# Optimization experiments

Hardware: AMD Instinct MI355X
Metric: run time of the kernel (lower is better)

## Reference

```python
import jax, jax.numpy as jnp
import numpy as np

N_TREES, N_LEAVES, PATH_LEN, N_NODES, D, B = 10, 16, 5, 31, 256, 4096


def _local_paths():
    # root-to-leaf paths of a full binary tree, depth 4: 31 nodes, 16 leaves, path len 5
    return np.array([[0, 1 + l // 8, 3 + l // 4, 7 + l // 2, 15 + l]
                     for l in range(N_LEAVES)], np.int32)


def setup_inputs() -> dict:
    key = jax.random.key(0)
    k1, k2, k3, k4, k5, k6 = jax.random.split(key, 6)
    # one activated leaf per tree -> multi-hot cross_features (B, N_TREES*N_LEAVES)
    leaf = jax.random.randint(k1, (B, N_TREES), 0, N_LEAVES)
    cross = jnp.zeros((B, N_TREES, N_LEAVES), jnp.float32)
    cross = cross.at[jnp.arange(B)[:, None], jnp.arange(N_TREES)[None, :], leaf].set(1.0)
    cross_features = cross.reshape(B, N_TREES * N_LEAVES)
    # learned params: node embedding table + single-layer LSTM (torch init scale 1/sqrt(D))
    emb = jax.random.normal(k2, (N_TREES * N_NODES, D), jnp.float32) * 0.02
    s = 1.0 / np.sqrt(D)
    W_ih = jax.random.uniform(k3, (4 * D, D), jnp.float32, -s, s)
    W_hh = jax.random.uniform(k4, (4 * D, D), jnp.float32, -s, s)
    b_ih = jax.random.uniform(k5, (4 * D,), jnp.float32, -s, s)
    b_hh = jax.random.uniform(k6, (4 * D,), jnp.float32, -s, s)
    return {"cross_features": cross_features, "emb": emb, "W_ih": W_ih,
            "W_hh": W_hh, "b_ih": b_ih, "b_hh": b_hh}


def reference(cross_features, emb, W_ih, W_hh, b_ih, b_hh):
    # global path node ids per (tree, leaf): [T, L, P]
    gpaths = jnp.asarray(_local_paths())[None, :, :] + \
        (jnp.arange(N_TREES, dtype=jnp.int32) * N_NODES)[:, None, None]
    # activated leaf per tree (exactly one hot per 16-leaf block)
    leaf = jnp.argmax(cross_features.reshape(B, N_TREES, N_LEAVES), axis=-1)  # [B, T]
    node_ids = gpaths[jnp.arange(N_TREES)[None, :], leaf]                     # [B, T, P]
    x = emb[node_ids].reshape(B * N_TREES, PATH_LEN, D)                       # packed paths
    # precompute input projections for all steps: [N, P, 4D]
    xg = jnp.einsum('npd,gd->npg', x, W_ih) + (b_ih + b_hh)

    def step(carry, xt):
        h, c = carry
        g = xt + h @ W_hh.T
        i, f, gg, o = jnp.split(g, 4, axis=-1)  # torch gate order: i, f, g, o
        c = jax.nn.sigmoid(f) * c + jax.nn.sigmoid(i) * jnp.tanh(gg)
        h = jax.nn.sigmoid(o) * jnp.tanh(c)
        return (h, c), None

    n = B * N_TREES
    h0 = jnp.zeros((n, D), x.dtype)
    (h, _), _ = jax.lax.scan(step, (h0, h0), jnp.swapaxes(xg, 0, 1))
    return h.reshape(B, N_TREES, D)
```

## Files before the change

kernel.cpp:

```cpp
#include <hip/hip_runtime.h>

#define NT 10
#define NL 16
#define NN 31
#define DD 256
#define NB 4096

__device__ unsigned g_gen[NT * 16];

__device__ __forceinline__ float sigf(float x)   { return 1.0f / (1.0f + __expf(-x)); }
__device__ __forceinline__ float tanh_f(float x) { return 2.0f / (1.0f + __expf(-2.0f*x)) - 1.0f; }

__device__ __forceinline__ void pub64(unsigned long long* p, unsigned tag, float v) {
    union { float f; unsigned u; } c; c.f = v;
    __hip_atomic_store(p, ((unsigned long long)tag << 32) | c.u,
                       __ATOMIC_RELAXED, __HIP_MEMORY_SCOPE_AGENT);
}
__device__ __forceinline__ unsigned long long ld64(const unsigned long long* p) {
    return __hip_atomic_load(p, __ATOMIC_RELAXED, __HIP_MEMORY_SCOPE_AGENT);
}
__device__ __forceinline__ float payload(unsigned long long w) {
    union { unsigned u; float f; } c; c.u = (unsigned)w; return c.f;
}

__global__ __launch_bounds__(256) void k_treelstm(
    const float* __restrict__ emb, const float* __restrict__ Wih,
    const float* __restrict__ Whh, const float* __restrict__ bih,
    const float* __restrict__ bhh,
    unsigned long long* __restrict__ hx0, unsigned long long* __restrict__ hx1,
    unsigned long long* __restrict__ hx2, unsigned long long* __restrict__ hx3,
    float* __restrict__ h4g)
{
    __shared__ float es [NN * DD];
    __shared__ float ps [8 * DD];
    __shared__ float xsl[NN * 64];
    __shared__ float hs [8 * DD];
    __shared__ float cbuf[2 * 128];
    __shared__ float bsl[64];
    __shared__ unsigned stag;

    const int tid  = threadIdx.x;
    const int t    = blockIdx.x >> 4;
    const int dt   = blockIdx.x & 15;
    const int kq   = tid >> 6;
    const int w    = tid & 63;
    const int gate = w >> 4;
    const int col  = w & 15;
    const int grow = gate * DD + dt * 16 + col;

    if (tid == 0) {
        unsigned G = __hip_atomic_load(&g_gen[t * 16 + dt],
            __ATOMIC_RELAXED, __HIP_MEMORY_SCOPE_AGENT);
        __hip_atomic_store(&g_gen[t * 16 + dt], G + 1u,
            __ATOMIC_RELAXED, __HIP_MEMORY_SCOPE_AGENT);
        stag = G + 1u;
    }
    if (tid < 64) {
        int g2 = tid >> 4, c3 = tid & 15;
        int r2 = g2 * DD + dt * 16 + c3;
        bsl[tid] = bih[r2] + bhh[r2];
    }

    const float4* Wi4 = (const float4*)Wih + (size_t)grow * 64 + kq * 16;
    const float4* Wh4 = (const float4*)Whh + (size_t)grow * 64 + kq * 16;
    float4 wih[16], whh[16];
    #pragma unroll
    for (int j = 0; j < 16; ++j) { wih[j] = Wi4[j]; whh[j] = Wh4[j]; }

    const float4* emb4 = (const float4*)emb + (size_t)t * NN * 64;
    float4* es4 = (float4*)es;
    #pragma unroll
    for (int r = 0; r < 8; ++r) {
        int idx = tid + 256 * r;
        if (idx < NN * 64) es4[idx] = emb4[idx];
    }
    __syncthreads();
    const unsigned tag = stag;

    auto xbatch = [&](int n0, int nn) {
        __syncthreads();
        float acc[8];
        #pragma unroll
        for (int m = 0; m < 8; ++m) acc[m] = 0.f;
        #pragma unroll
        for (int j = 0; j < 16; ++j) {
            float4 wv = wih[j];
            #pragma unroll
            for (int m = 0; m < 8; ++m) {
                if (m < nn) {
                    float4 h = es4[(n0 + m) * 64 + kq * 16 + j];
                    acc[m] = fmaf(wv.x, h.x, fmaf(wv.y, h.y,
                             fmaf(wv.z, h.z, fmaf(wv.w, h.w, acc[m]))));
                }
            }
        }
        #pragma unroll
        for (int m = 0; m < 8; ++m)
            if (m < nn) ps[m * DD + kq * 64 + w] = acc[m];
        __syncthreads();
        #pragma unroll
        for (int rep = 0; rep < 2; ++rep) {
            int idx = tid + 256 * rep;
            if (idx < nn * 64) {
                int m = idx >> 6, w2 = idx & 63;
                xsl[(n0 + m) * 64 + w2] =
                      ps[m * DD +   0 + w2] + ps[m * DD +  64 + w2]
                    + ps[m * DD + 128 + w2] + ps[m * DD + 192 + w2] + bsl[w2];
            }
        }
        __syncthreads();
    };

    xbatch(0, 1);
    if (tid < 16) {
        float xi  = xsl[ 0 + tid];
        float xgg = xsl[32 + tid];
        float xo  = xsl[48 + tid];
        float c0 = sigf(xi) * tanh_f(xgg);
        float h0 = sigf(xo) * tanh_f(c0);
        cbuf[tid] = c0;
        pub64(hx0 + (size_t)t * DD + dt * 16 + tid, tag, h0);
    }

    xbatch(1, 6);

    {
        const unsigned long long* src = hx0 + (size_t)t * DD;
        unsigned long long v = ld64(src + tid);
        while ((unsigned)(v >> 32) != tag) {
            __builtin_amdgcn_s_sleep(1);
            v = ld64(src + tid);
        }
        hs[tid] = payload(v);
    }
    __syncthreads();

    const unsigned long long* hin[3] = { hx1, hx2, hx3 };
    unsigned long long* hout[3] = { hx1, hx2, hx3 };

    #pragma unroll
    for (int s = 1; s <= 4; ++s) {
        const int L = 1 << (s - 1);

        if (s > 1) {
            const unsigned long long* src = hin[s - 2] + (size_t)t * L * DD;
            unsigned long long v[8];
            #pragma unroll
            for (int r = 0; r < L; ++r) v[r] = ld64(src + tid + 256 * r);
            #pragma unroll
            for (int r = 0; r < L; ++r) {
                while ((unsigned)(v[r] >> 32) != tag) {
                    __builtin_amdgcn_s_sleep(1);
                    v[r] = ld64(src + tid + 256 * r);
                }
                hs[tid + 256 * r] = payload(v[r]);
            }
            __syncthreads();
        }

        const float4* hs4 = (const float4*)hs;
        float acc[8];
        #pragma unroll
        for (int p = 0; p < 8; ++p) acc[p] = 0.f;
        #pragma unroll
        for (int j = 0; j < 16; ++j) {
            float4 wv = whh[j];
            #pragma unroll
            for (int p = 0; p < L; ++p) {
                float4 h = hs4[p * 64 + kq * 16 + j];
                acc[p] = fmaf(wv.x, h.x, fmaf(wv.y, h.y,
                         fmaf(wv.z, h.z, fmaf(wv.w, h.w, acc[p]))));
            }
        }
        #pragma unroll
        for (int p = 0; p < L; ++p) ps[p * DD + kq * 64 + w] = acc[p];
        __syncthreads();

        if (tid < 32 * L) {
            const int p  = tid >> 5;
            const int c2 = tid & 15;
            const int q  = tid >> 4;
            float g0 = 0.f, g1 = 0.f, g2 = 0.f, g3 = 0.f;
            #pragma unroll
            for (int k = 0; k < 4; ++k) {
                const float* pp = ps + p * DD + k * 64;
                g0 += pp[ 0 + c2]; g1 += pp[16 + c2];
                g2 += pp[32 + c2]; g3 += pp[48 + c2];
            }
            const int node = (1 << s) - 1 + q;
            const float* xp = xsl + node * 64;
            float gi = g0 + xp[ 0 + c2];
            float gf = g1 + xp[16 + c2];
            float gg = g2 + xp[32 + c2];
            float go = g3 + xp[48 + c2];
            float cin = cbuf[((s - 1) & 1) * 128 + p * 16 + c2];
            float cn  = sigf(gf) * cin + sigf(gi) * tanh_f(gg);
            float hn  = sigf(go) * tanh_f(cn);
            if (s < 4) {
                cbuf[(s & 1) * 128 + q * 16 + c2] = cn;
                pub64(hout[s - 1] + (size_t)(t * 2 * L + q) * DD
                                  + dt * 16 + c2, tag, hn);
            } else {
                h4g[(size_t)(t * NL + q) * DD + dt * 16 + c2] = hn;
            }
        }

        if (s == 1)      xbatch( 7, 8);
        else if (s == 2) xbatch(15, 8);
        else if (s == 3) xbatch(23, 8);
    }
}

__global__ __launch_bounds__(256) void k_scatter(
    const float* __restrict__ cross, const float* __restrict__ htab,
    float* __restrict__ out)
{
    const int tid  = threadIdx.x;
    const int wave = tid >> 6;
    const int lane = tid & 63;
    const int r0 = (blockIdx.x * 4 + wave) * 4;

    float v = cross[(size_t)r0 * NL + lane];
    unsigned long long m = __ballot(v > 0.5f);

    const int g  = lane >> 4;
    const int rr = r0 + g;
    const int b  = rr / NT;
    const int t  = rr - b * NT;
    unsigned mg = (unsigned)(m >> (g * 16)) & 0xFFFFu;
    int leaf = mg ? (int)__builtin_ctz(mg) : 0;
    int p = t * NL + leaf;

    const float4* h4 = (const float4*)htab;
    float4* o4 = (float4*)out;

    #pragma unroll
    for (int it = 0; it < 4; ++it) {
        int pit = __shfl(p, it * 16);
        o4[(size_t)(r0 + it) * 64 + lane] = h4[(size_t)pit * 64 + lane];
    }
}

extern "C" void kernel_launch(void* const* d_in, const int* in_sizes, int n_in,
                              void* d_out, int out_size, void* d_ws, size_t ws_size,
                              hipStream_t stream)
{
    const float* cross = (const float*)d_in[0];
    const float* emb   = (const float*)d_in[1];
    const float* Wih   = (const float*)d_in[2];
    const float* Whh   = (const float*)d_in[3];
    const float* bih   = (const float*)d_in[4];
    const float* bhh   = (const float*)d_in[5];
    float* out = (float*)d_out;

    unsigned long long* hx0 = (unsigned long long*)d_ws;
    unsigned long long* hx1 = hx0 + (size_t)NT * DD;
    unsigned long long* hx2 = hx1 + (size_t)2 * NT * DD;
    unsigned long long* hx3 = hx2 + (size_t)4 * NT * DD;
    float* h4g = (float*)(hx3 + (size_t)8 * NT * DD);

    hipLaunchKernelGGL(k_treelstm, dim3(160), dim3(256), 0, stream,
                       emb, Wih, Whh, bih, bhh, hx0, hx1, hx2, hx3, h4g);
    hipLaunchKernelGGL(k_scatter, dim3(2560), dim3(256), 0, stream,
                       cross, h4g, out);
}
```

Measured before the change: 100.8 us.

## Fuse leaf scatter into tree-LSTM kernel, overlapping leaf decoding with recurrence

Removes the separate scatter kernel. Each tree-LSTM block now decodes the activated leaf for all 4096 batch rows of its tree, in chunks interleaved with the recurrence steps. After the last step it writes its 16-column slice of the leaf hidden states straight to the output. This drops one launch and the global round-trip of the leaf hidden-state table. In exchange, only 160 blocks write all 42 MB of output, with 64-byte strided stores per row, and every block rereads the cross features for its tree (16 blocks per tree).

```diff
diff --git a/kernel.cpp b/kernel.cpp
--- a/kernel.cpp
+++ b/kernel.cpp
@@ -24,12 +24,12 @@
 }
 
 __global__ __launch_bounds__(256) void k_treelstm(
-    const float* __restrict__ emb, const float* __restrict__ Wih,
-    const float* __restrict__ Whh, const float* __restrict__ bih,
-    const float* __restrict__ bhh,
+    const float* __restrict__ cross, const float* __restrict__ emb,
+    const float* __restrict__ Wih,   const float* __restrict__ Whh,
+    const float* __restrict__ bih,   const float* __restrict__ bhh,
     unsigned long long* __restrict__ hx0, unsigned long long* __restrict__ hx1,
     unsigned long long* __restrict__ hx2, unsigned long long* __restrict__ hx3,
-    float* __restrict__ h4g)
+    float* __restrict__ out)
 {
     __shared__ float es [NN * DD];
     __shared__ float ps [8 * DD];
@@ -37,6 +37,8 @@
     __shared__ float hs [8 * DD];
     __shared__ float cbuf[2 * 128];
     __shared__ float bsl[64];
+    __shared__ float h4f[NL * 16];
+    __shared__ unsigned char leafs[NB];
     __shared__ unsigned stag;
 
     const int tid  = threadIdx.x;
@@ -109,6 +111,28 @@
             }
         }
         __syncthreads();
+    };
+
+    const float4* cf4 = (const float4*)cross;
+    auto leafchunk = [&](int b0) {
+        #pragma unroll
+        for (int r = 0; r < 4; ++r) {
+            int b = b0 + r * 256 + tid;
+            float4 q0 = cf4[(size_t)b * 40 + t * 4 + 0];
+            float4 q1 = cf4[(size_t)b * 40 + t * 4 + 1];
+            float4 q2 = cf4[(size_t)b * 40 + t * 4 + 2];
+            float4 q3 = cf4[(size_t)b * 40 + t * 4 + 3];
+            int lf = 0;
+            if (q3.w > 0.5f) lf = 15; if (q3.z > 0.5f) lf = 14;
+            if (q3.y > 0.5f) lf = 13; if (q3.x > 0.5f) lf = 12;
+            if (q2.w > 0.5f) lf = 11; if (q2.z > 0.5f) lf = 10;
+            if (q2.y > 0.5f) lf =  9; if (q2.x > 0.5f) lf =  8;
+            if (q1.w > 0.5f) lf =  7; if (q1.z > 0.5f) lf =  6;
+            if (q1.y > 0.5f) lf =  5; if (q1.x > 0.5f) lf =  4;
+            if (q0.w > 0.5f) lf =  3; if (q0.z > 0.5f) lf =  2;
+            if (q0.y > 0.5f) lf =  1; if (q0.x > 0.5f) lf =  0;
+            leafs[b] = (unsigned char)lf;
+        }
     };
 
     xbatch(0, 1);
@@ -123,6 +147,7 @@
     }
 
     xbatch(1, 6);
+    leafchunk(0);
 
     {
         const unsigned long long* src = hx0 + (size_t)t * DD;
@@ -201,43 +226,25 @@
                 pub64(hout[s - 1] + (size_t)(t * 2 * L + q) * DD
                                   + dt * 16 + c2, tag, hn);
             } else {
-                h4g[(size_t)(t * NL + q) * DD + dt * 16 + c2] = hn;
-            }
-        }
-
-        if (s == 1)      xbatch( 7, 8);
-        else if (s == 2) xbatch(15, 8);
-        else if (s == 3) xbatch(23, 8);
-    }
-}
-
-__global__ __launch_bounds__(256) void k_scatter(
-    const float* __restrict__ cross, const float* __restrict__ htab,
-    float* __restrict__ out)
-{
-    const int tid  = threadIdx.x;
-    const int wave = tid >> 6;
-    const int lane = tid & 63;
-    const int r0 = (blockIdx.x * 4 + wave) * 4;
-
-    float v = cross[(size_t)r0 * NL + lane];
-    unsigned long long m = __ballot(v > 0.5f);
-
-    const int g  = lane >> 4;
-    const int rr = r0 + g;
-    const int b  = rr / NT;
-    const int t  = rr - b * NT;
-    unsigned mg = (unsigned)(m >> (g * 16)) & 0xFFFFu;
-    int leaf = mg ? (int)__builtin_ctz(mg) : 0;
-    int p = t * NL + leaf;
-
-    const float4* h4 = (const float4*)htab;
+                h4f[q * 16 + c2] = hn;
+            }
+        }
+
+        if (s == 1)      { xbatch( 7, 8); leafchunk(1024); }
+        else if (s == 2) { xbatch(15, 8); leafchunk(2048); }
+        else if (s == 3) { xbatch(23, 8); leafchunk(3072); }
+    }
+    __syncthreads();
+
+    const float4* h44 = (const float4*)h4f;
     float4* o4 = (float4*)out;
-
-    #pragma unroll
-    for (int it = 0; it < 4; ++it) {
-        int pit = __shfl(p, it * 16);
-        o4[(size_t)(r0 + it) * 64 + lane] = h4[(size_t)pit * 64 + lane];
+    const int c4 = tid & 3;
+    const int bb = tid >> 2;
+    #pragma unroll 4
+    for (int i = 0; i < 64; ++i) {
+        int b = i * 64 + bb;
+        int lf = leafs[b];
+        o4[((size_t)b * NT + t) * 64 + dt * 4 + c4] = h44[lf * 4 + c4];
     }
 }
 
@@ -257,10 +264,8 @@
     unsigned long long* hx1 = hx0 + (size_t)NT * DD;
     unsigned long long* hx2 = hx1 + (size_t)2 * NT * DD;
     unsigned long long* hx3 = hx2 + (size_t)4 * NT * DD;
-    float* h4g = (float*)(hx3 + (size_t)8 * NT * DD);
 
     hipLaunchKernelGGL(k_treelstm, dim3(160), dim3(256), 0, stream,
-                       emb, Wih, Whh, bih, bhh, hx0, hx1, hx2, hx3, h4g);
-    hipLaunchKernelGGL(k_scatter, dim3(2560), dim3(256), 0, stream,
-                       cross, h4g, out);
-}
+                       cross, emb, Wih, Whh, bih, bhh,
+                       hx0, hx1, hx2, hx3, out);
+}
```

Result: slower. 139.6 us (+38.5%).
